# Kernel optimization log

Measured on AMD Instinct MI355X. Metric: run time of the kernel, lower is better.

## Reference

```python
import jax, jax.numpy as jnp
import numpy as np

H = 1024        # hidden_size
E = 32          # moe_num_experts
I = 512         # moe_intermediate_size
TOP_K = 6       # moe_k
IS = 1024       # shared intermediate = I * num_shared_experts
NORM_MIN = 1e-12
B, S = 2, 1024


def setup_inputs() -> dict:
    key = jax.random.key(0)
    ks = jax.random.split(key, 8)
    sc = 0.02  # realistic init scale for weights
    return {
        "hidden_states": jax.random.normal(ks[0], (B, S, H), jnp.float32),
        "router_weight": jax.random.normal(ks[1], (E, H), jnp.float32) * sc,
        "e_score_bias": jnp.zeros((E,), jnp.float32),
        "gate_up_proj": jax.random.normal(ks[2], (E, 2 * I, H), jnp.float32) * sc,
        "down_proj": jax.random.normal(ks[3], (E, H, I), jnp.float32) * sc,
        "shared_gate_w": jax.random.normal(ks[4], (IS, H), jnp.float32) * sc,
        "shared_up_w": jax.random.normal(ks[5], (IS, H), jnp.float32) * sc,
        "shared_down_w": jax.random.normal(ks[6], (H, IS), jnp.float32) * sc,
    }


def reference(hidden_states, router_weight, e_score_bias, gate_up_proj, down_proj,
              shared_gate_w, shared_up_w, shared_down_w):
    b, s, h = hidden_states.shape
    x = hidden_states.reshape(-1, h)                      # [T, H]
    T = x.shape[0]

    # shared experts: SiLU-gated MLP
    shared_out = (jax.nn.silu(x @ shared_gate_w.T) * (x @ shared_up_w.T)) @ shared_down_w.T

    # router (fp32, autocast disabled in original)
    xf = x.astype(jnp.float32)
    router_logits = xf @ router_weight.T                  # [T, E]
    routing_weights = jax.nn.softmax(router_logits, axis=-1)
    corrected = routing_weights + e_score_bias            # moe_statics bias
    _, top_idx = jax.lax.top_k(corrected, TOP_K)          # [T, K]
    top_w = jnp.take_along_axis(routing_weights, top_idx, axis=-1)
    top_w = top_w / jnp.clip(top_w.sum(axis=-1, keepdims=True), NORM_MIN)
    top_w = top_w.astype(x.dtype)

    # combine weights per expert via scatter-add (equivalent to one-hot dispatch)
    combine = jnp.zeros((T, E), x.dtype).at[jnp.arange(T)[:, None], top_idx].add(top_w)

    # dense grouped expert MLP (same math as per-expert gather/GEMM/scatter)
    gu = jnp.einsum('th,eih->tei', x, gate_up_proj)       # [T, E, 2I]
    gate, up = jnp.split(gu, 2, axis=-1)
    hmid = jax.nn.silu(gate) * up                         # [T, E, I]
    y = jnp.einsum('tei,ehi->teh', hmid, down_proj)       # [T, E, H]
    out = jnp.einsum('teh,te->th', y, combine) + shared_out
    return out.reshape(b, s, h)
```

## Files before the change

kernel.cpp:

```cpp
#include <hip/hip_runtime.h>
#include <stdint.h>

#define HDIM 1024
#define NEXP 32
#define IDIM 512
#define TOPK 6
#define NTOK 2048
#define NPAIR (NTOK*TOPK)

typedef __attribute__((ext_vector_type(4))) float f32x4;
typedef __attribute__((ext_vector_type(8))) short s16x8;
typedef __attribute__((ext_vector_type(8))) __bf16 bf16x8;

static __device__ __forceinline__ f32x4 mfma16(s16x8 a, s16x8 b, f32x4 c){
  return __builtin_amdgcn_mfma_f32_16x16x32_bf16(
      __builtin_bit_cast(bf16x8, a), __builtin_bit_cast(bf16x8, b), c, 0, 0, 0);
}

static __device__ __forceinline__ short bf1(float f){
  return __builtin_bit_cast(short, (__bf16)f);
}
static __device__ __forceinline__ s16x8 pack8v(f32x4 a, f32x4 b){
  bf16x8 o;
  o[0]=(__bf16)a[0]; o[1]=(__bf16)a[1]; o[2]=(__bf16)a[2]; o[3]=(__bf16)a[3];
  o[4]=(__bf16)b[0]; o[5]=(__bf16)b[1]; o[6]=(__bf16)b[2]; o[7]=(__bf16)b[3];
  return __builtin_bit_cast(s16x8, o);
}

#define GLL16(SRC, DST) __builtin_amdgcn_global_load_lds( \
    (const __attribute__((address_space(1))) void*)(SRC), \
    (__attribute__((address_space(3))) void*)(DST), 16, 0, 0)

static __device__ __forceinline__ void wait_vm8(){
  asm volatile("s_waitcnt vmcnt(8)" ::: "memory");
  __builtin_amdgcn_sched_barrier(0);
}
static __device__ __forceinline__ void wait_vm0(){
  asm volatile("s_waitcnt vmcnt(0)" ::: "memory");
  __builtin_amdgcn_sched_barrier(0);
}
static __device__ __forceinline__ void barrier_raw(){
  __builtin_amdgcn_sched_barrier(0);
  __builtin_amdgcn_s_barrier();
  __builtin_amdgcn_sched_barrier(0);
}

static __device__ __forceinline__ s16x8 frag_ld(const short* lds, int row, int ks, int lane){
  int kb  = ks*64 + ((lane >> 4) << 4);
  int off = row*128 + (kb ^ ((row & 7) << 4));
  return *(const s16x8*)(lds + (off >> 1));
}

__global__ __launch_bounds__(256) void k_convert_router(const float* __restrict__ gu,
    const float* __restrict__ dn, const float* __restrict__ sg,
    const float* __restrict__ su, const float* __restrict__ sd,
    short* __restrict__ bgu, short* __restrict__ bdn, short* __restrict__ bsg,
    short* __restrict__ bsu, short* __restrict__ bsd,
    const float* __restrict__ x, const float* __restrict__ rw,
    const float* __restrict__ bias, short* __restrict__ xb,
    int* __restrict__ tki, float* __restrict__ tkw, int* __restrict__ counts){
  int b = blockIdx.x;
  if (b >= 512){
    int cb = b - 512;
    const float* src; short* dst; long base;
    if (cb < 2048)      { src=gu;  dst=bgu; base=(long)cb*2048; }
    else if (cb < 3072) { src=dn;  dst=bdn; base=(long)(cb-2048)*2048; }
    else if (cb < 3136) { src=sg;  dst=bsg; base=(long)(cb-3072)*2048; }
    else if (cb < 3200) { src=su;  dst=bsu; base=(long)(cb-3136)*2048; }
    else                { src=sd;  dst=bsd; base=(long)(cb-3200)*2048; }
    const f32x4* s4 = (const f32x4*)src;
    long i0 = base + threadIdx.x;
    f32x4 la[8], lc[8];
    #pragma unroll
    for (int it = 0; it < 8; ++it){
      long i = i0 + (long)it*256;
      la[it] = __builtin_nontemporal_load(s4 + 2*i);
      lc[it] = __builtin_nontemporal_load(s4 + 2*i + 1);
    }
    #pragma unroll
    for (int it = 0; it < 8; ++it){
      long i = i0 + (long)it*256;
      *(s16x8*)(dst + 8*i) = pack8v(la[it], lc[it]);
    }
    return;
  }
  if (b == 0 && threadIdx.x < NEXP) counts[threadIdx.x] = 0;
  int wid = threadIdx.x >> 6, lane = threadIdx.x & 63;
  int t = b*4 + wid;
  const f32x4* xr4 = (const f32x4*)(x + (long)t*HDIM);
  f32x4 xv[4];
  #pragma unroll
  for (int j = 0; j < 4; ++j) xv[j] = xr4[lane + j*64];
  #pragma unroll
  for (int j = 0; j < 4; ++j){
    short4 o; o.x = bf1(xv[j][0]); o.y = bf1(xv[j][1]); o.z = bf1(xv[j][2]); o.w = bf1(xv[j][3]);
    *(short4*)(xb + (long)t*HDIM + (lane + j*64)*4) = o;
  }
  float mylogit = -1e30f;
  #pragma unroll 8
  for (int e = 0; e < NEXP; ++e){
    const f32x4* wr4 = (const f32x4*)(rw + (long)e*HDIM);
    f32x4 acc = xv[0]*wr4[lane];
    acc += xv[1]*wr4[lane + 64];
    acc += xv[2]*wr4[lane + 128];
    acc += xv[3]*wr4[lane + 192];
    float s = acc[0] + acc[1] + acc[2] + acc[3];
    #pragma unroll
    for (int sh = 32; sh; sh >>= 1) s += __shfl_xor(s, sh);
    if (lane == e) mylogit = s;
  }
  float m = mylogit;
  #pragma unroll
  for (int sh = 32; sh; sh >>= 1) m = fmaxf(m, __shfl_xor(m, sh));
  float p = (lane < NEXP) ? __expf(mylogit - m) : 0.f;
  float sum = p;
  #pragma unroll
  for (int sh = 32; sh; sh >>= 1) sum += __shfl_xor(sum, sh);
  p = p / sum;
  float rem = (lane < NEXP) ? (p + bias[lane]) : -1e30f;
  int myidx = 0; float myw = 0.f;
  for (int k = 0; k < TOPK; ++k){
    float vv = rem; int ix = lane;
    #pragma unroll
    for (int sh = 32; sh; sh >>= 1){
      float ov = __shfl_xor(vv, sh); int oi = __shfl_xor(ix, sh);
      if (ov > vv || (ov == vv && oi < ix)){ vv = ov; ix = oi; }
    }
    float pw = __shfl(p, ix);
    if (lane == ix) rem = -1e30f;
    if (lane == k){ myidx = ix; myw = pw; }
  }
  float s6 = (lane < TOPK) ? myw : 0.f;
  #pragma unroll
  for (int sh = 32; sh; sh >>= 1) s6 += __shfl_xor(s6, sh);
  if (lane < TOPK){
    tki[t*TOPK + lane] = myidx;
    tkw[t*TOPK + lane] = myw / fmaxf(s6, 1e-12f);
  }
}

__global__ __launch_bounds__(256) void k_hist(const int* __restrict__ tki,
                                              int* __restrict__ counts){
  __shared__ int h[NEXP];
  int tid = threadIdx.x;
  if (tid < NEXP) h[tid] = 0;
  __syncthreads();
  #pragma unroll
  for (int j = 0; j < 4; ++j)
    atomicAdd(&h[tki[blockIdx.x*1024 + j*256 + tid]], 1);
  __syncthreads();
  if (tid < NEXP) atomicAdd(&counts[tid], h[tid]);
}

__global__ void k_scan(const int* __restrict__ counts, int* __restrict__ offsets,
                       int* __restrict__ cursor){
  if (threadIdx.x == 0){
    int s = 0;
    for (int e = 0; e < NEXP; ++e){ offsets[e] = s; cursor[e] = s; s += counts[e]; }
    offsets[NEXP] = s;
  }
}

__global__ __launch_bounds__(256) void k_scatter(const int* __restrict__ tki,
    const float* __restrict__ tkw, int* __restrict__ cursor,
    int* __restrict__ permt, float* __restrict__ permw, int* __restrict__ pairpos){
  __shared__ int lcnt[NEXP], lbase[NEXP];
  int tid = threadIdx.x;
  if (tid < NEXP) lcnt[tid] = 0;
  __syncthreads();
  int e[4], lr[4];
  #pragma unroll
  for (int j = 0; j < 4; ++j){
    int i = blockIdx.x*1024 + j*256 + tid;
    e[j] = tki[i];
    lr[j] = atomicAdd(&lcnt[e[j]], 1);
  }
  __syncthreads();
  if (tid < NEXP) lbase[tid] = atomicAdd(&cursor[tid], lcnt[tid]);
  __syncthreads();
  #pragma unroll
  for (int j = 0; j < 4; ++j){
    int i = blockIdx.x*1024 + j*256 + tid;
    int pos = lbase[e[j]] + lr[j];
    permt[pos] = i / TOPK;
    permw[pos] = tkw[i];
    pairpos[i] = pos;
  }
}

__global__ __launch_bounds__(256,2) void k_gu(const short* __restrict__ xb,
    const short* __restrict__ bgu, const short* __restrict__ bsg,
    const short* __restrict__ bsu, const int* __restrict__ offsets,
    const int* __restrict__ permt, short* __restrict__ hmid, short* __restrict__ sb){
  bool expert = (blockIdx.z >= 2);
  int tid = threadIdx.x, lane = tid & 63, wid = tid >> 6, wr = wid >> 1, wc = wid & 1;
  __shared__ short As[2][128*64];
  __shared__ short Bg[2][64*64];
  __shared__ short Bu[2][64*64];
  __shared__ int rowmap[128];
  int m0 = blockIdx.y*128, n0;
  int off = 0, seg = NTOK;
  const short *wg, *wu;
  if (expert){
    int e = blockIdx.z - 2;
    off = offsets[e]; seg = offsets[e+1] - off;
    if (m0 >= seg) return;
    n0 = blockIdx.x*64;
    wg = bgu + (long)e*1024*HDIM + (long)n0*HDIM;
    wu = wg + (long)IDIM*HDIM;
    if (tid < 128) rowmap[tid] = permt[off + min(m0 + tid, seg - 1)];
  } else {
    n0 = blockIdx.z*512 + blockIdx.x*64;
    wg = bsg + (long)n0*HDIM;
    wu = bsu + (long)n0*HDIM;
    if (tid < 128) rowmap[tid] = m0 + tid;
  }
  __syncthreads();
  const short* aS[4]; int aD[4];
  #pragma unroll
  for (int p = 0; p < 4; ++p){
    int c = p*256 + tid, row = c >> 3;
    int skb = ((c & 7) << 4) ^ ((row & 7) << 4);
    aS[p] = xb + (long)rowmap[row]*HDIM + (skb >> 1);
    aD[p] = c*8;
  }
  const short *gS[2], *uS[2]; int bD[2];
  #pragma unroll
  for (int p = 0; p < 2; ++p){
    int c = p*256 + tid, row = c >> 3;
    int skb = ((c & 7) << 4) ^ ((row & 7) << 4);
    gS[p] = wg + (long)row*HDIM + (skb >> 1);
    uS[p] = wu + (long)row*HDIM + (skb >> 1);
    bD[p] = c*8;
  }
  auto ISSUE = [&](int kt_, int buf){
    int k0 = kt_*64;
    #pragma unroll
    for (int p = 0; p < 4; ++p) GLL16(aS[p]+k0, &As[buf][aD[p]]);
    #pragma unroll
    for (int p = 0; p < 2; ++p){ GLL16(gS[p]+k0, &Bg[buf][bD[p]]); GLL16(uS[p]+k0, &Bu[buf][bD[p]]); }
  };
  f32x4 z = {0.f,0.f,0.f,0.f};
  f32x4 ag[4][2], au[4][2];
  for (int i=0;i<4;i++) for (int j=0;j<2;j++){ ag[i][j]=z; au[i][j]=z; }
  const int nkt = HDIM/64;
  ISSUE(0, 0);
  ISSUE(1, 1);
  wait_vm8();
  barrier_raw();
  int cur = 0;
  for (int kt = 0; kt < nkt; ++kt){
    #pragma unroll
    for (int ks = 0; ks < 2; ++ks){
      s16x8 af[4], g2[2], u2[2];
      #pragma unroll
      for (int i = 0; i < 4; ++i) af[i] = frag_ld(&As[cur][0], wr*64 + i*16 + (lane&15), ks, lane);
      #pragma unroll
      for (int j = 0; j < 2; ++j){
        g2[j] = frag_ld(&Bg[cur][0], wc*32 + j*16 + (lane&15), ks, lane);
        u2[j] = frag_ld(&Bu[cur][0], wc*32 + j*16 + (lane&15), ks, lane);
      }
      #pragma unroll
      for (int i = 0; i < 4; ++i)
        #pragma unroll
        for (int j = 0; j < 2; ++j){
          ag[i][j] = mfma16(af[i], g2[j], ag[i][j]);
          au[i][j] = mfma16(af[i], u2[j], au[i][j]);
        }
    }
    barrier_raw();
    if (kt + 2 < nkt){
      ISSUE(kt + 2, cur);
      wait_vm8();
      barrier_raw();
    } else if (kt + 1 < nkt){
      wait_vm0();
      barrier_raw();
    }
    cur ^= 1;
  }
  #pragma unroll
  for (int i = 0; i < 4; ++i){
    int mrow = wr*64 + i*16 + ((lane >> 4) << 2);
    #pragma unroll
    for (int j = 0; j < 2; ++j){
      int col = n0 + wc*32 + j*16 + (lane & 15);
      #pragma unroll
      for (int r = 0; r < 4; ++r){
        int m = mrow + r;
        float gv = ag[i][j][r], uv = au[i][j][r];
        float sv = gv / (1.f + __expf(-gv)) * uv;
        if (expert){
          if (m0 + m < seg)
            hmid[(long)(off + m0 + m)*IDIM + col] = bf1(sv);
        } else {
          sb[(long)(m0 + m)*1024 + col] = bf1(sv);
        }
      }
    }
  }
}

__global__ __launch_bounds__(256,2) void k_down(const short* __restrict__ hmid,
    const short* __restrict__ bdn, const short* __restrict__ sb,
    const short* __restrict__ bsd, const int* __restrict__ offsets,
    const int* __restrict__ permt, const float* __restrict__ permw,
    short* __restrict__ y, float* __restrict__ out){
  bool expert = (blockIdx.z >= 1);
  int tid = threadIdx.x, lane = tid & 63, wid = tid >> 6, wr = wid >> 1, wc = wid & 1;
  __shared__ short As[2][128*64];
  __shared__ short Bs[2][128*64];
  __shared__ int rowmap[128];
  int m0 = blockIdx.y*128, n0 = blockIdx.x*128;
  int off = 0, seg = NTOK, nkt, lda, ldb;
  const short* Ag; const short* Bgp;
  if (expert){
    int e = blockIdx.z - 1;
    off = offsets[e]; seg = offsets[e+1] - off;
    if (m0 >= seg) return;
    Ag = hmid; lda = IDIM;
    Bgp = bdn + (long)e*HDIM*IDIM + (long)n0*IDIM; ldb = IDIM;
    nkt = IDIM/64;
    if (tid < 128) rowmap[tid] = off + min(m0 + tid, seg - 1);
  } else {
    Ag = sb; lda = 1024;
    Bgp = bsd + (long)n0*1024; ldb = 1024;
    nkt = 1024/64;
    if (tid < 128) rowmap[tid] = m0 + tid;
  }
  __syncthreads();
  const short *aS[4], *bS[4]; int cD[4];
  #pragma unroll
  for (int p = 0; p < 4; ++p){
    int c = p*256 + tid, row = c >> 3;
    int skb = ((c & 7) << 4) ^ ((row & 7) << 4);
    aS[p] = Ag + (long)rowmap[row]*lda + (skb >> 1);
    bS[p] = Bgp + (long)row*ldb + (skb >> 1);
    cD[p] = c*8;
  }
  auto ISSUE = [&](int kt_, int buf){
    int k0 = kt_*64;
    #pragma unroll
    for (int p = 0; p < 4; ++p){ GLL16(aS[p]+k0, &As[buf][cD[p]]); GLL16(bS[p]+k0, &Bs[buf][cD[p]]); }
  };
  f32x4 z = {0.f,0.f,0.f,0.f};
  f32x4 acc[4][4];
  for (int i=0;i<4;i++) for (int j=0;j<4;j++) acc[i][j]=z;
  ISSUE(0, 0);
  ISSUE(1, 1);
  wait_vm8();
  barrier_raw();
  int cur = 0;
  for (int kt = 0; kt < nkt; ++kt){
    #pragma unroll
    for (int ks = 0; ks < 2; ++ks){
      s16x8 af[4], bf[4];
      #pragma unroll
      for (int i = 0; i < 4; ++i){
        af[i] = frag_ld(&As[cur][0], wr*64 + i*16 + (lane&15), ks, lane);
        bf[i] = frag_ld(&Bs[cur][0], wc*64 + i*16 + (lane&15), ks, lane);
      }
      #pragma unroll
      for (int i = 0; i < 4; ++i)
        #pragma unroll
        for (int j = 0; j < 4; ++j)
          acc[i][j] = mfma16(af[i], bf[j], acc[i][j]);
    }
    barrier_raw();
    if (kt + 2 < nkt){
      ISSUE(kt + 2, cur);
      wait_vm8();
      barrier_raw();
    } else if (kt + 1 < nkt){
      wait_vm0();
      barrier_raw();
    }
    cur ^= 1;
  }
  if (expert){
    #pragma unroll
    for (int i = 0; i < 4; ++i){
      int mrow = wr*64 + i*16 + ((lane >> 4) << 2);
      #pragma unroll
      for (int r = 0; r < 4; ++r){
        int m = mrow + r;
        if (m0 + m < seg){
          int p = off + m0 + m;
          float w = permw[p];
          #pragma unroll
          for (int j = 0; j < 4; ++j){
            int col = n0 + wc*64 + j*16 + (lane & 15);
            y[(long)p*HDIM + col] = bf1(w*acc[i][j][r]);
          }
        }
      }
    }
  } else {
    #pragma unroll
    for (int i = 0; i < 4; ++i){
      int mrow = m0 + wr*64 + i*16 + ((lane >> 4) << 2);
      #pragma unroll
      for (int j = 0; j < 4; ++j){
        int col = n0 + wc*64 + j*16 + (lane & 15);
        #pragma unroll
        for (int r = 0; r < 4; ++r)
          out[(long)(mrow + r)*HDIM + col] = acc[i][j][r];
      }
    }
  }
}

__global__ __launch_bounds__(256) void k_finalize(const short* __restrict__ y,
    const int* __restrict__ pairpos, float* __restrict__ out){
  int t = blockIdx.x, tid = threadIdx.x;
  const int* pp = pairpos + t*TOPK;
  float4* o4 = (float4*)(out + (long)t*HDIM);
  float4 acc = o4[tid];
  #pragma unroll
  for (int k = 0; k < TOPK; ++k){
    const short4 v = *(const short4*)(y + (long)pp[k]*HDIM + tid*4);
    acc.x += (float)__builtin_bit_cast(__bf16, v.x);
    acc.y += (float)__builtin_bit_cast(__bf16, v.y);
    acc.z += (float)__builtin_bit_cast(__bf16, v.z);
    acc.w += (float)__builtin_bit_cast(__bf16, v.w);
  }
  o4[tid] = acc;
}

extern "C" void kernel_launch(void* const* d_in, const int* in_sizes, int n_in,
                              void* d_out, int out_size, void* d_ws, size_t ws_size,
                              hipStream_t stream){
  const float* x    = (const float*)d_in[0];
  const float* rw   = (const float*)d_in[1];
  const float* bias = (const float*)d_in[2];
  const float* wgu  = (const float*)d_in[3];
  const float* wdn  = (const float*)d_in[4];
  const float* wsg  = (const float*)d_in[5];
  const float* wsu  = (const float*)d_in[6];
  const float* wsd  = (const float*)d_in[7];
  float* out = (float*)d_out;

  char* ws = (char*)d_ws;
  size_t o = 0;
  auto alloc = [&](size_t bytes){ void* p = ws + o; o += (bytes + 255) & ~(size_t)255; return p; };
  short* bgu  = (short*)alloc(67108864);
  short* bdn  = (short*)alloc(33554432);
  short* bsg  = (short*)alloc(2097152);
  short* bsu  = (short*)alloc(2097152);
  short* bsd  = (short*)alloc(2097152);
  short* xb   = (short*)alloc(4194304);
  short* sb   = (short*)alloc(4194304);
  short* hmid = (short*)alloc(12582912);
  int*   tki  = (int*)alloc(NPAIR*4);
  float* tkw  = (float*)alloc(NPAIR*4);
  int*   counts  = (int*)alloc(256);
  int*   offsets = (int*)alloc(256);
  int*   cursor  = (int*)alloc(256);
  int*   permt   = (int*)alloc(NPAIR*4);
  float* permw   = (float*)alloc(NPAIR*4);
  int*   pairpos = (int*)alloc(NPAIR*4);
  short* y = (short*)bgu;
  (void)ws_size; (void)in_sizes; (void)n_in; (void)out_size;

  k_convert_router<<<dim3(512 + 3264), dim3(256), 0, stream>>>(
      wgu, wdn, wsg, wsu, wsd, bgu, bdn, bsg, bsu, bsd,
      x, rw, bias, xb, tki, tkw, counts);
  k_hist<<<dim3(NPAIR/1024), dim3(256), 0, stream>>>(tki, counts);
  k_scan<<<dim3(1), dim3(64), 0, stream>>>(counts, offsets, cursor);
  k_scatter<<<dim3(NPAIR/1024), dim3(256), 0, stream>>>(tki, tkw, cursor, permt, permw, pairpos);
  k_gu<<<dim3(8, 16, NEXP+2), dim3(256), 0, stream>>>(xb, bgu, bsg, bsu, offsets, permt, hmid, sb);
  k_down<<<dim3(8, 16, NEXP+1), dim3(256), 0, stream>>>(hmid, bdn, sb, bsd, offsets, permt, permw, y, out);
  k_finalize<<<dim3(NTOK), dim3(256), 0, stream>>>(y, pairpos, out);
}
```

Baseline: 187.3 us.

## Move down-proj weight conversion into gate-up kernel to overlap with GEMM

Measured after the change: 183.2 us. 1.02x faster.

```diff
diff --git a/kernel.cpp b/kernel.cpp
--- a/kernel.cpp
+++ b/kernel.cpp
@@ -51,10 +51,28 @@
   return *(const s16x8*)(lds + (off >> 1));
 }
 
+static __device__ __forceinline__ void conv_slab(const float* __restrict__ src,
+                                                 short* __restrict__ dst, long cb, int tid){
+  const f32x4* s4 = (const f32x4*)src;
+  long i0 = cb*2048 + tid;
+  f32x4 la[8], lc[8];
+  #pragma unroll
+  for (int it = 0; it < 8; ++it){
+    long i = i0 + (long)it*256;
+    la[it] = __builtin_nontemporal_load(s4 + 2*i);
+    lc[it] = __builtin_nontemporal_load(s4 + 2*i + 1);
+  }
+  #pragma unroll
+  for (int it = 0; it < 8; ++it){
+    long i = i0 + (long)it*256;
+    *(s16x8*)(dst + 8*i) = pack8v(la[it], lc[it]);
+  }
+}
+
 __global__ __launch_bounds__(256) void k_convert_router(const float* __restrict__ gu,
-    const float* __restrict__ dn, const float* __restrict__ sg,
-    const float* __restrict__ su, const float* __restrict__ sd,
-    short* __restrict__ bgu, short* __restrict__ bdn, short* __restrict__ bsg,
+    const float* __restrict__ sg, const float* __restrict__ su,
+    const float* __restrict__ sd,
+    short* __restrict__ bgu, short* __restrict__ bsg,
     short* __restrict__ bsu, short* __restrict__ bsd,
     const float* __restrict__ x, const float* __restrict__ rw,
     const float* __restrict__ bias, short* __restrict__ xb,
@@ -62,26 +80,10 @@
   int b = blockIdx.x;
   if (b >= 512){
     int cb = b - 512;
-    const float* src; short* dst; long base;
-    if (cb < 2048)      { src=gu;  dst=bgu; base=(long)cb*2048; }
-    else if (cb < 3072) { src=dn;  dst=bdn; base=(long)(cb-2048)*2048; }
-    else if (cb < 3136) { src=sg;  dst=bsg; base=(long)(cb-3072)*2048; }
-    else if (cb < 3200) { src=su;  dst=bsu; base=(long)(cb-3136)*2048; }
-    else                { src=sd;  dst=bsd; base=(long)(cb-3200)*2048; }
-    const f32x4* s4 = (const f32x4*)src;
-    long i0 = base + threadIdx.x;
-    f32x4 la[8], lc[8];
-    #pragma unroll
-    for (int it = 0; it < 8; ++it){
-      long i = i0 + (long)it*256;
-      la[it] = __builtin_nontemporal_load(s4 + 2*i);
-      lc[it] = __builtin_nontemporal_load(s4 + 2*i + 1);
-    }
-    #pragma unroll
-    for (int it = 0; it < 8; ++it){
-      long i = i0 + (long)it*256;
-      *(s16x8*)(dst + 8*i) = pack8v(la[it], lc[it]);
-    }
+    if (cb < 2048)      conv_slab(gu, bgu, cb, threadIdx.x);
+    else if (cb < 2112) conv_slab(sg, bsg, cb - 2048, threadIdx.x);
+    else if (cb < 2176) conv_slab(su, bsu, cb - 2112, threadIdx.x);
+    else                conv_slab(sd, bsd, cb - 2176, threadIdx.x);
     return;
   }
   if (b == 0 && threadIdx.x < NEXP) counts[threadIdx.x] = 0;
@@ -191,9 +193,17 @@
 __global__ __launch_bounds__(256,2) void k_gu(const short* __restrict__ xb,
     const short* __restrict__ bgu, const short* __restrict__ bsg,
     const short* __restrict__ bsu, const int* __restrict__ offsets,
-    const int* __restrict__ permt, short* __restrict__ hmid, short* __restrict__ sb){
-  bool expert = (blockIdx.z >= 2);
-  int tid = threadIdx.x, lane = tid & 63, wid = tid >> 6, wr = wid >> 1, wc = wid & 1;
+    const int* __restrict__ permt, short* __restrict__ hmid, short* __restrict__ sb,
+    const float* __restrict__ wdnf, short* __restrict__ bdn){
+  int zz = blockIdx.z;
+  int tid = threadIdx.x;
+  if (zz >= 2 && zz < 10){
+    long cb = (long)(zz - 2)*128 + blockIdx.y*8 + blockIdx.x;
+    conv_slab(wdnf, bdn, cb, tid);
+    return;
+  }
+  bool expert = (zz >= 10);
+  int lane = tid & 63, wid = tid >> 6, wr = wid >> 1, wc = wid & 1;
   __shared__ short As[2][128*64];
   __shared__ short Bg[2][64*64];
   __shared__ short Bu[2][64*64];
@@ -202,7 +212,7 @@
   int off = 0, seg = NTOK;
   const short *wg, *wu;
   if (expert){
-    int e = blockIdx.z - 2;
+    int e = zz - 10;
     off = offsets[e]; seg = offsets[e+1] - off;
     if (m0 >= seg) return;
     n0 = blockIdx.x*64;
@@ -210,7 +220,7 @@
     wu = wg + (long)IDIM*HDIM;
     if (tid < 128) rowmap[tid] = permt[off + min(m0 + tid, seg - 1)];
   } else {
-    n0 = blockIdx.z*512 + blockIdx.x*64;
+    n0 = zz*512 + blockIdx.x*64;
     wg = bsg + (long)n0*HDIM;
     wu = bsu + (long)n0*HDIM;
     if (tid < 128) rowmap[tid] = m0 + tid;
@@ -462,13 +472,14 @@
   short* y = (short*)bgu;
   (void)ws_size; (void)in_sizes; (void)n_in; (void)out_size;
 
-  k_convert_router<<<dim3(512 + 3264), dim3(256), 0, stream>>>(
-      wgu, wdn, wsg, wsu, wsd, bgu, bdn, bsg, bsu, bsd,
+  k_convert_router<<<dim3(512 + 2240), dim3(256), 0, stream>>>(
+      wgu, wsg, wsu, wsd, bgu, bsg, bsu, bsd,
       x, rw, bias, xb, tki, tkw, counts);
   k_hist<<<dim3(NPAIR/1024), dim3(256), 0, stream>>>(tki, counts);
   k_scan<<<dim3(1), dim3(64), 0, stream>>>(counts, offsets, cursor);
   k_scatter<<<dim3(NPAIR/1024), dim3(256), 0, stream>>>(tki, tkw, cursor, permt, permw, pairpos);
-  k_gu<<<dim3(8, 16, NEXP+2), dim3(256), 0, stream>>>(xb, bgu, bsg, bsu, offsets, permt, hmid, sb);
+  k_gu<<<dim3(8, 16, NEXP+10), dim3(256), 0, stream>>>(xb, bgu, bsg, bsu, offsets, permt,
+                                                       hmid, sb, wdn, bdn);
   k_down<<<dim3(8, 16, NEXP+1), dim3(256), 0, stream>>>(hmid, bdn, sb, bsd, offsets, permt, permw, y, out);
   k_finalize<<<dim3(NTOK), dim3(256), 0, stream>>>(y, pairpos, out);
 }
```
